# Kernel optimization log

Hardware: AMD Instinct MI355X
Metric: run time of the kernel (lower is better)

The kernel has to match this reference:

```python
import jax, jax.numpy as jnp
import numpy as np

N_NODES = 100000
N_EDGES = 1000000
D_IN = 64
D_OUT = 64


def setup_inputs() -> dict:
    key = jax.random.key(0)
    k_x, k_e, k_w, k_b = jax.random.split(key, 4)
    x = jax.random.normal(k_x, (N_NODES, D_IN), dtype=jnp.float32)
    edge_index = jax.random.randint(k_e, (2, N_EDGES), 0, N_NODES, dtype=jnp.int64)
    # degrees of destination nodes (what the caller is expected to supply);
    # clamp to >=1 to avoid division by zero for isolated nodes
    deg = jax.ops.segment_sum(jnp.ones((N_EDGES,), jnp.float32), edge_index[1], num_segments=N_NODES)
    node_degrees = jnp.maximum(deg, 1.0)
    W = jax.random.normal(k_w, (D_OUT, D_IN), dtype=jnp.float32) * (1.0 / np.sqrt(D_IN))
    b = jax.random.normal(k_b, (D_OUT,), dtype=jnp.float32) * 0.01
    return {"x": x, "edge_index": edge_index, "node_degrees": node_degrees, "W": W, "b": b}


def reference(x, edge_index, node_degrees, W, b):
    # Original does argsort+cumsum+boundary segment-sum; mathematically this is
    # a scatter-add of gathered neighbor features into dst, i.e. a segment sum.
    src, dst = edge_index[0], edge_index[1]
    agg = jax.ops.segment_sum(x[src], dst, num_segments=x.shape[0])  # [N, D_IN]
    mean = agg / node_degrees[:, None]
    return mean @ W.T + b  # [N, D_OUT]
```

## Files before the change

### kernel.cpp

```cpp
#include <hip/hip_runtime.h>


#define D 64
#define BSHIFT 7
#define BNODES (1 << BSHIFT)
#define CAP 2048
#define GTHREADS 512
#define PERTHREAD (CAP / GTHREADS)
#define PXW_THREADS 512
#define MAXB 2048

__device__ inline int detect_stride_block(const unsigned* __restrict__ words,
                                          int E, int* sflag) {
    int t = threadIdx.x;
    if (t < 64) {
        unsigned v = (t < E) ? words[2 * t + 1] : 0u;
        int any = __any(v != 0u);
        if (t == 0) *sflag = any ? 1 : 2;
    }
    __syncthreads();
    return *sflag;
}

__device__ inline unsigned pack_bf16(float a, float b) {
    unsigned ua = __float_as_uint(a), ub = __float_as_uint(b);
    ua += 0x7fffu + ((ua >> 16) & 1u);
    ub += 0x7fffu + ((ub >> 16) & 1u);
    return (ua >> 16) | (ub & 0xffff0000u);
}

__global__ __launch_bounds__(PXW_THREADS, 4) void partition_xw_kernel(
        const unsigned* __restrict__ ewords, int* __restrict__ cursor,
        unsigned* __restrict__ pairs, uint2* __restrict__ spill,
        int* __restrict__ spillCnt,
        const float* __restrict__ x, const float* __restrict__ W,
        unsigned* __restrict__ y2, int E, int N, int nb, int pblocks) {
    __shared__ __align__(16) char smem[52240];
    int t = threadIdx.x;

    if ((int)blockIdx.x < pblocks) {
        int* lhist = (int*)smem;
        int* lbase = lhist + MAXB;
        int* sflag = lbase + MAXB;
        int s = detect_stride_block(ewords, E, sflag);
        int base = blockIdx.x * 8192;
        for (int i = t; i < nb; i += PXW_THREADS) lhist[i] = 0;
        __syncthreads();
        unsigned pv[16]; int bk[16];
        #pragma unroll
        for (int k = 0; k < 16; ++k) {
            int e = base + k * PXW_THREADS + t;
            bk[k] = -1;
            if (e < E) {
                unsigned src = ewords[(size_t)e * s];
                unsigned dst = ewords[((size_t)E + e) * s];
                bk[k] = (int)(dst >> BSHIFT);
                pv[k] = src | ((dst & (BNODES - 1)) << 17);
                atomicAdd(&lhist[bk[k]], 1);
            }
        }
        __syncthreads();
        for (int hb = t; hb < nb; hb += PXW_THREADS) {
            int cc = lhist[hb];
            if (cc) lbase[hb] = atomicAdd(&cursor[hb], cc);
            lhist[hb] = 0;
        }
        __syncthreads();
        #pragma unroll
        for (int k = 0; k < 16; ++k) {
            if (bk[k] >= 0) {
                int lpos = lbase[bk[k]] + atomicAdd(&lhist[bk[k]], 1);
                if (lpos < CAP) {
                    pairs[(size_t)bk[k] * CAP + lpos] = pv[k];
                } else {
                    int si = atomicAdd(spillCnt, 1);
                    unsigned dst = ((unsigned)bk[k] << BSHIFT) | (pv[k] >> 17);
                    spill[si] = make_uint2(pv[k] & 0x1FFFFu, dst);
                }
            }
        }
    } else {
        float* Wt = (float*)smem;
        float* xs = Wt + 64 * 68;
        for (int i = t; i < 64 * 64; i += PXW_THREADS) {
            int o = i >> 6, k = i & 63;
            Wt[k * 68 + o] = W[i];
        }
        int base = ((int)blockIdx.x - pblocks) * 128;
        int row = t >> 4, c4 = (t & 15) * 4;
        #pragma unroll
        for (int r = 0; r < 4; ++r) {
            int nl = row + r * 32;
            int n = base + nl;
            float4 v = {0.f, 0.f, 0.f, 0.f};
            if (n < N) v = *(const float4*)(x + (size_t)n * 64 + c4);
            *(float4*)&xs[nl * 68 + c4] = v;
        }
        __syncthreads();
        int o4 = (t & 15) * 4, nl4 = (t >> 4) * 4;
        float acc[4][4];
        #pragma unroll
        for (int i = 0; i < 4; ++i)
            #pragma unroll
            for (int j = 0; j < 4; ++j) acc[i][j] = 0.f;
        #pragma unroll 2
        for (int k0 = 0; k0 < 64; k0 += 4) {
            float a[4][4], wv[4][4];
            #pragma unroll
            for (int i = 0; i < 4; ++i)
                *(float4*)a[i] = *(const float4*)&xs[(nl4 + i) * 68 + k0];
            #pragma unroll
            for (int dk = 0; dk < 4; ++dk)
                *(float4*)wv[dk] = *(const float4*)&Wt[(k0 + dk) * 68 + o4];
            #pragma unroll
            for (int i = 0; i < 4; ++i)
                #pragma unroll
                for (int j = 0; j < 4; ++j)
                    acc[i][j] += a[i][0] * wv[0][j] + a[i][1] * wv[1][j]
                               + a[i][2] * wv[2][j] + a[i][3] * wv[3][j];
        }
        int n0 = base + nl4;
        #pragma unroll
        for (int i = 0; i < 4; ++i) {
            if (n0 + i < N) {
                uint2 p;
                p.x = pack_bf16(acc[i][0], acc[i][1]);
                p.y = pack_bf16(acc[i][2], acc[i][3]);
                *(uint2*)(y2 + (size_t)(n0 + i) * 32 + (o4 >> 1)) = p;
            }
        }
    }
}

__global__ __launch_bounds__(GTHREADS) void bucket_gather(
        const unsigned* __restrict__ y2, const unsigned* __restrict__ pairs,
        const int* __restrict__ cursor, const uint2* __restrict__ spill,
        const int* __restrict__ spillCnt,
        const float* __restrict__ deg, const float* __restrict__ b,
        float* __restrict__ out, int N) {
    __shared__ unsigned list[CAP];
    __shared__ int cnt[BNODES], st[BNODES], sc[BNODES];
    int t = threadIdx.x;
    int bkt = blockIdx.x, base = bkt << BSHIFT;
    int total = cursor[bkt];
    int cn = total < CAP ? total : CAP;
    int lane = t & 63, w = t >> 6;
    int g = lane >> 4, c = lane & 15;
    float4 bv = ((const float4*)b)[c];

    if (t < BNODES) cnt[t] = 0;
    __syncthreads();
    unsigned pv[PERTHREAD];
    #pragma unroll
    for (int j = 0; j < PERTHREAD; ++j) {
        int i = t + j * GTHREADS;
        pv[j] = (i < cn) ? pairs[(size_t)bkt * CAP + i] : 0xFFFFFFFFu;
        if (i < cn) atomicAdd(&cnt[pv[j] >> 17], 1);
    }
    __syncthreads();
    if (t < BNODES) sc[t] = cnt[t];
    __syncthreads();
    for (int off = 1; off < BNODES; off <<= 1) {
        int v = (t < BNODES && t >= off) ? sc[t - off] : 0;
        __syncthreads();
        if (t < BNODES) sc[t] += v;
        __syncthreads();
    }
    if (t < BNODES) { st[t] = sc[t] - cnt[t]; sc[t] = sc[t] - cnt[t]; }
    __syncthreads();
    #pragma unroll
    for (int j = 0; j < PERTHREAD; ++j) {
        if (pv[j] != 0xFFFFFFFFu) {
            int pos = atomicAdd(&sc[pv[j] >> 17], 1);
            list[pos] = pv[j] & 0x1FFFFu;
        }
    }
    __syncthreads();

    int scnt = *spillCnt;

    for (int nl0 = w * 16; nl0 < w * 16 + 16; nl0 += 4) {
        int mynode = nl0 + g;
        int n = base + mynode;
        int s0 = st[mynode], e1 = s0 + cnt[mynode];
        float ax = 0.f, ay = 0.f, az = 0.f, aw = 0.f;
        float bx = 0.f, by = 0.f, bz = 0.f, bw = 0.f;
        int i = s0;
        for (; i + 1 < e1; i += 2) {
            unsigned s0v = list[i], s1v = list[i + 1];
            uint2 u0 = *(const uint2*)(y2 + (size_t)s0v * 32 + c * 2);
            uint2 u1 = *(const uint2*)(y2 + (size_t)s1v * 32 + c * 2);
            ax += __uint_as_float(u0.x << 16);
            ay += __uint_as_float(u0.x & 0xffff0000u);
            az += __uint_as_float(u0.y << 16);
            aw += __uint_as_float(u0.y & 0xffff0000u);
            bx += __uint_as_float(u1.x << 16);
            by += __uint_as_float(u1.x & 0xffff0000u);
            bz += __uint_as_float(u1.y << 16);
            bw += __uint_as_float(u1.y & 0xffff0000u);
        }
        if (i < e1) {
            unsigned sv = list[i];
            uint2 u = *(const uint2*)(y2 + (size_t)sv * 32 + c * 2);
            ax += __uint_as_float(u.x << 16);
            ay += __uint_as_float(u.x & 0xffff0000u);
            az += __uint_as_float(u.y << 16);
            aw += __uint_as_float(u.y & 0xffff0000u);
        }
        ax += bx; ay += by; az += bz; aw += bw;
        for (int k = 0; k < scnt; ++k) {
            uint2 e = spill[k];
            if ((int)e.y == n) {
                uint2 u = *(const uint2*)(y2 + (size_t)e.x * 32 + c * 2);
                ax += __uint_as_float(u.x << 16);
                ay += __uint_as_float(u.x & 0xffff0000u);
                az += __uint_as_float(u.y << 16);
                aw += __uint_as_float(u.y & 0xffff0000u);
            }
        }
        if (n < N) {
            float invd = 1.0f / deg[n];
            float4 o4 = {ax * invd + bv.x, ay * invd + bv.y,
                         az * invd + bv.z, aw * invd + bv.w};
            *(float4*)(out + (size_t)n * 64 + c * 4) = o4;
        }
    }
}

__global__ __launch_bounds__(256) void scatter_kernel(
        const float* __restrict__ x, const unsigned* __restrict__ ewords,
        float* __restrict__ agg, int E) {
    __shared__ int sflag;
    int s = detect_stride_block(ewords, E, &sflag);
    int gid = blockIdx.x * blockDim.x + threadIdx.x;
    int e = gid >> 4, q = gid & 15;
    if (e >= E) return;
    int src = (int)ewords[(size_t)e * s];
    int dst = (int)ewords[((size_t)E + e) * s];
    const float4 v = *(const float4*)(x + (size_t)src * D + q * 4);
    float* p = agg + (size_t)dst * D + q * 4;
    unsafeAtomicAdd(p + 0, v.x);
    unsafeAtomicAdd(p + 1, v.y);
    unsafeAtomicAdd(p + 2, v.z);
    unsafeAtomicAdd(p + 3, v.w);
}

__global__ __launch_bounds__(256) void gemm_kernel(
        float* __restrict__ inout, const float* __restrict__ deg,
        const float* __restrict__ W, const float* __restrict__ b, int nNodes) {
    __shared__ float Wt[64 * 65];
    __shared__ float rows[4 * 64];
    int t = threadIdx.x;
    for (int i = t; i < 64 * 64; i += 256) {
        int o = i >> 6, k = i & 63;
        Wt[k * 65 + o] = W[i];
    }
    int base = blockIdx.x * 4;
    int nl = t >> 6, o = t & 63;
    int n = base + nl;
    if (n < nNodes) {
        float invd = 1.0f / deg[n];
        rows[nl * 64 + o] = inout[(size_t)n * 64 + o] * invd;
    }
    __syncthreads();
    if (n >= nNodes) return;
    float acc = b[o];
    #pragma unroll
    for (int k = 0; k < 64; ++k)
        acc += rows[nl * 64 + k] * Wt[k * 65 + o];
    inout[(size_t)n * 64 + o] = acc;
}

extern "C" void kernel_launch(void* const* d_in, const int* in_sizes, int n_in,
                              void* d_out, int out_size, void* d_ws, size_t ws_size,
                              hipStream_t stream) {
    const float*    x      = (const float*)d_in[0];
    const unsigned* ewords = (const unsigned*)d_in[1];
    const float*    deg    = (const float*)d_in[2];
    const float*    W      = (const float*)d_in[3];
    const float*    b      = (const float*)d_in[4];
    float*          out    = (float*)d_out;

    const int E = in_sizes[1] / 2;
    const int N = in_sizes[2];
    const int nb = (N + BNODES - 1) >> BSHIFT;

    char* ws = (char*)d_ws;
    size_t curB  = (MAXB + 16) * 4;
    size_t pairB = ((size_t)nb * CAP * 4 + 63) & ~63ull;
    size_t spB   = ((size_t)E * 8 + 63) & ~63ull;
    size_t need  = curB + pairB + spB + (size_t)N * 32 * 4;

    if (ws_size >= need && N < (1 << 17) && nb <= MAXB) {
        int*      cursor   = (int*)ws;
        int*      spillCnt = cursor + MAXB;
        unsigned* pairs    = (unsigned*)(ws + curB);
        uint2*    spill    = (uint2*)(ws + curB + pairB);
        unsigned* y2       = (unsigned*)(ws + curB + pairB + spB);

        hipMemsetAsync(cursor, 0, curB, stream);

        int pblocks  = (E + 8191) / 8192;
        int xwblocks = (N + 127) / 128;
        partition_xw_kernel<<<pblocks + xwblocks, PXW_THREADS, 0, stream>>>(
            ewords, cursor, pairs, spill, spillCnt, x, W, y2, E, N, nb, pblocks);

        bucket_gather<<<nb, GTHREADS, 0, stream>>>(
            y2, pairs, cursor, spill, spillCnt, deg, b, out, N);
    } else {
        hipMemsetAsync(d_out, 0, (size_t)out_size * sizeof(float), stream);
        long long sthreads = (long long)E * 16;
        int sblocks = (int)((sthreads + 255) / 256);
        scatter_kernel<<<sblocks, 256, 0, stream>>>(x, ewords, out, E);
        gemm_kernel<<<(N + 3) / 4, 256, 0, stream>>>(out, deg, W, b, N);
    }
}
```

Before: 139.8 us.

## Shrink gather buckets to 32 nodes with one 16-lane group per node

Bucket size drops from 128 to 32 nodes and per-bucket capacity from 2048 to 512 edges, so each of the 512 threads holds exactly one pair. Each 16-lane group now owns a single node instead of looping over four, and the shared-memory prefix scan over node counts becomes a single-wave shuffle scan. The aim is more, smaller blocks with fewer barriers and more parallelism in the gather. The risk is that a per-bucket capacity of 512 sits close to the expected ~320 edges per bucket, so overflows into the spill list (which every thread scans linearly) may become more frequent. MAXB rises to cover the larger bucket count.

Result: no change. 142.0 us (+1.6%).

```diff
diff --git a/kernel.cpp b/kernel.cpp
--- a/kernel.cpp
+++ b/kernel.cpp
@@ -2,13 +2,12 @@
 
 
 #define D 64
-#define BSHIFT 7
+#define BSHIFT 5
 #define BNODES (1 << BSHIFT)
-#define CAP 2048
+#define CAP 512
 #define GTHREADS 512
-#define PERTHREAD (CAP / GTHREADS)
 #define PXW_THREADS 512
-#define MAXB 2048
+#define MAXB 3328
 
 __device__ inline int detect_stride_block(const unsigned* __restrict__ words,
                                           int E, int* sflag) {
@@ -144,86 +143,74 @@
     int bkt = blockIdx.x, base = bkt << BSHIFT;
     int total = cursor[bkt];
     int cn = total < CAP ? total : CAP;
-    int lane = t & 63, w = t >> 6;
-    int g = lane >> 4, c = lane & 15;
+    int node = t >> 4, c = t & 15;
     float4 bv = ((const float4*)b)[c];
 
     if (t < BNODES) cnt[t] = 0;
     __syncthreads();
-    unsigned pv[PERTHREAD];
-    #pragma unroll
-    for (int j = 0; j < PERTHREAD; ++j) {
-        int i = t + j * GTHREADS;
-        pv[j] = (i < cn) ? pairs[(size_t)bkt * CAP + i] : 0xFFFFFFFFu;
-        if (i < cn) atomicAdd(&cnt[pv[j] >> 17], 1);
-    }
-    __syncthreads();
-    if (t < BNODES) sc[t] = cnt[t];
-    __syncthreads();
-    for (int off = 1; off < BNODES; off <<= 1) {
-        int v = (t < BNODES && t >= off) ? sc[t - off] : 0;
-        __syncthreads();
-        if (t < BNODES) sc[t] += v;
-        __syncthreads();
-    }
-    if (t < BNODES) { st[t] = sc[t] - cnt[t]; sc[t] = sc[t] - cnt[t]; }
-    __syncthreads();
-    #pragma unroll
-    for (int j = 0; j < PERTHREAD; ++j) {
-        if (pv[j] != 0xFFFFFFFFu) {
-            int pos = atomicAdd(&sc[pv[j] >> 17], 1);
-            list[pos] = pv[j] & 0x1FFFFu;
-        }
+    unsigned pv = (t < cn) ? pairs[(size_t)bkt * CAP + t] : 0xFFFFFFFFu;
+    if (pv != 0xFFFFFFFFu) atomicAdd(&cnt[pv >> 17], 1);
+    __syncthreads();
+    if (t < 64) {
+        int v = (t < BNODES) ? cnt[t] : 0;
+        #pragma unroll
+        for (int off = 1; off < BNODES; off <<= 1) {
+            int u = __shfl_up(v, off);
+            if ((t & 63) >= off) v += u;
+        }
+        if (t < BNODES) { st[t] = v - cnt[t]; sc[t] = v - cnt[t]; }
+    }
+    __syncthreads();
+    if (pv != 0xFFFFFFFFu) {
+        int pos = atomicAdd(&sc[pv >> 17], 1);
+        list[pos] = pv & 0x1FFFFu;
     }
     __syncthreads();
 
     int scnt = *spillCnt;
 
-    for (int nl0 = w * 16; nl0 < w * 16 + 16; nl0 += 4) {
-        int mynode = nl0 + g;
-        int n = base + mynode;
-        int s0 = st[mynode], e1 = s0 + cnt[mynode];
-        float ax = 0.f, ay = 0.f, az = 0.f, aw = 0.f;
-        float bx = 0.f, by = 0.f, bz = 0.f, bw = 0.f;
-        int i = s0;
-        for (; i + 1 < e1; i += 2) {
-            unsigned s0v = list[i], s1v = list[i + 1];
-            uint2 u0 = *(const uint2*)(y2 + (size_t)s0v * 32 + c * 2);
-            uint2 u1 = *(const uint2*)(y2 + (size_t)s1v * 32 + c * 2);
-            ax += __uint_as_float(u0.x << 16);
-            ay += __uint_as_float(u0.x & 0xffff0000u);
-            az += __uint_as_float(u0.y << 16);
-            aw += __uint_as_float(u0.y & 0xffff0000u);
-            bx += __uint_as_float(u1.x << 16);
-            by += __uint_as_float(u1.x & 0xffff0000u);
-            bz += __uint_as_float(u1.y << 16);
-            bw += __uint_as_float(u1.y & 0xffff0000u);
-        }
-        if (i < e1) {
-            unsigned sv = list[i];
-            uint2 u = *(const uint2*)(y2 + (size_t)sv * 32 + c * 2);
+    int n = base + node;
+    int s0 = st[node], e1 = s0 + cnt[node];
+    float ax = 0.f, ay = 0.f, az = 0.f, aw = 0.f;
+    float bx = 0.f, by = 0.f, bz = 0.f, bw = 0.f;
+    int i = s0;
+    for (; i + 1 < e1; i += 2) {
+        unsigned s0v = list[i], s1v = list[i + 1];
+        uint2 u0 = *(const uint2*)(y2 + (size_t)s0v * 32 + c * 2);
+        uint2 u1 = *(const uint2*)(y2 + (size_t)s1v * 32 + c * 2);
+        ax += __uint_as_float(u0.x << 16);
+        ay += __uint_as_float(u0.x & 0xffff0000u);
+        az += __uint_as_float(u0.y << 16);
+        aw += __uint_as_float(u0.y & 0xffff0000u);
+        bx += __uint_as_float(u1.x << 16);
+        by += __uint_as_float(u1.x & 0xffff0000u);
+        bz += __uint_as_float(u1.y << 16);
+        bw += __uint_as_float(u1.y & 0xffff0000u);
+    }
+    if (i < e1) {
+        unsigned sv = list[i];
+        uint2 u = *(const uint2*)(y2 + (size_t)sv * 32 + c * 2);
+        ax += __uint_as_float(u.x << 16);
+        ay += __uint_as_float(u.x & 0xffff0000u);
+        az += __uint_as_float(u.y << 16);
+        aw += __uint_as_float(u.y & 0xffff0000u);
+    }
+    ax += bx; ay += by; az += bz; aw += bw;
+    for (int k = 0; k < scnt; ++k) {
+        uint2 e = spill[k];
+        if ((int)e.y == n) {
+            uint2 u = *(const uint2*)(y2 + (size_t)e.x * 32 + c * 2);
             ax += __uint_as_float(u.x << 16);
             ay += __uint_as_float(u.x & 0xffff0000u);
             az += __uint_as_float(u.y << 16);
             aw += __uint_as_float(u.y & 0xffff0000u);
         }
-        ax += bx; ay += by; az += bz; aw += bw;
-        for (int k = 0; k < scnt; ++k) {
-            uint2 e = spill[k];
-            if ((int)e.y == n) {
-                uint2 u = *(const uint2*)(y2 + (size_t)e.x * 32 + c * 2);
-                ax += __uint_as_float(u.x << 16);
-                ay += __uint_as_float(u.x & 0xffff0000u);
-                az += __uint_as_float(u.y << 16);
-                aw += __uint_as_float(u.y & 0xffff0000u);
-            }
-        }
-        if (n < N) {
-            float invd = 1.0f / deg[n];
-            float4 o4 = {ax * invd + bv.x, ay * invd + bv.y,
-                         az * invd + bv.z, aw * invd + bv.w};
-            *(float4*)(out + (size_t)n * 64 + c * 4) = o4;
-        }
+    }
+    if (n < N) {
+        float invd = 1.0f / deg[n];
+        float4 o4 = {ax * invd + bv.x, ay * invd + bv.y,
+                     az * invd + bv.z, aw * invd + bv.w};
+        *(float4*)(out + (size_t)n * 64 + c * 4) = o4;
     }
 }
 
```

## Halve gather bucket size and widen per-thread loads to 16 bytes

Applied to the files above, without the earlier changes.

Buckets shrink from 128 to 64 destination nodes with capacity 1024, so twice as many blocks run the gather kernel. Each thread now handles one node and 8 channels with uint4 loads, eight threads per node, where before it looped over 4 nodes with uint2 loads. The shared-memory prefix scan over the 64 node counts becomes a single-wavefront shuffle scan, which drops several block-wide barriers. In exchange, high-degree nodes now sit on a single thread group, and the spill path may be hit more often when a bucket exceeds the smaller capacity.

After: 139.8 us. About the same (-0.0%).

```diff
diff --git a/kernel.cpp b/kernel.cpp
--- a/kernel.cpp
+++ b/kernel.cpp
@@ -2,9 +2,9 @@
 
 
 #define D 64
-#define BSHIFT 7
+#define BSHIFT 6
 #define BNODES (1 << BSHIFT)
-#define CAP 2048
+#define CAP 1024
 #define GTHREADS 512
 #define PERTHREAD (CAP / GTHREADS)
 #define PXW_THREADS 512
@@ -144,9 +144,9 @@
     int bkt = blockIdx.x, base = bkt << BSHIFT;
     int total = cursor[bkt];
     int cn = total < CAP ? total : CAP;
-    int lane = t & 63, w = t >> 6;
-    int g = lane >> 4, c = lane & 15;
-    float4 bv = ((const float4*)b)[c];
+    int node = t >> 3, c = t & 7;
+    float4 bv0 = ((const float4*)b)[c * 2];
+    float4 bv1 = ((const float4*)b)[c * 2 + 1];
 
     if (t < BNODES) cnt[t] = 0;
     __syncthreads();
@@ -155,18 +155,18 @@
     for (int j = 0; j < PERTHREAD; ++j) {
         int i = t + j * GTHREADS;
         pv[j] = (i < cn) ? pairs[(size_t)bkt * CAP + i] : 0xFFFFFFFFu;
-        if (i < cn) atomicAdd(&cnt[pv[j] >> 17], 1);
-    }
-    __syncthreads();
-    if (t < BNODES) sc[t] = cnt[t];
-    __syncthreads();
-    for (int off = 1; off < BNODES; off <<= 1) {
-        int v = (t < BNODES && t >= off) ? sc[t - off] : 0;
-        __syncthreads();
-        if (t < BNODES) sc[t] += v;
-        __syncthreads();
-    }
-    if (t < BNODES) { st[t] = sc[t] - cnt[t]; sc[t] = sc[t] - cnt[t]; }
+        if (pv[j] != 0xFFFFFFFFu) atomicAdd(&cnt[pv[j] >> 17], 1);
+    }
+    __syncthreads();
+    if (t < 64) {
+        int v = cnt[t];
+        #pragma unroll
+        for (int off = 1; off < 64; off <<= 1) {
+            int u = __shfl_up(v, off);
+            if (t >= off) v += u;
+        }
+        st[t] = v - cnt[t]; sc[t] = v - cnt[t];
+    }
     __syncthreads();
     #pragma unroll
     for (int j = 0; j < PERTHREAD; ++j) {
@@ -179,51 +179,70 @@
 
     int scnt = *spillCnt;
 
-    for (int nl0 = w * 16; nl0 < w * 16 + 16; nl0 += 4) {
-        int mynode = nl0 + g;
-        int n = base + mynode;
-        int s0 = st[mynode], e1 = s0 + cnt[mynode];
-        float ax = 0.f, ay = 0.f, az = 0.f, aw = 0.f;
-        float bx = 0.f, by = 0.f, bz = 0.f, bw = 0.f;
-        int i = s0;
-        for (; i + 1 < e1; i += 2) {
-            unsigned s0v = list[i], s1v = list[i + 1];
-            uint2 u0 = *(const uint2*)(y2 + (size_t)s0v * 32 + c * 2);
-            uint2 u1 = *(const uint2*)(y2 + (size_t)s1v * 32 + c * 2);
-            ax += __uint_as_float(u0.x << 16);
-            ay += __uint_as_float(u0.x & 0xffff0000u);
-            az += __uint_as_float(u0.y << 16);
-            aw += __uint_as_float(u0.y & 0xffff0000u);
-            bx += __uint_as_float(u1.x << 16);
-            by += __uint_as_float(u1.x & 0xffff0000u);
-            bz += __uint_as_float(u1.y << 16);
-            bw += __uint_as_float(u1.y & 0xffff0000u);
-        }
-        if (i < e1) {
-            unsigned sv = list[i];
-            uint2 u = *(const uint2*)(y2 + (size_t)sv * 32 + c * 2);
-            ax += __uint_as_float(u.x << 16);
-            ay += __uint_as_float(u.x & 0xffff0000u);
-            az += __uint_as_float(u.y << 16);
-            aw += __uint_as_float(u.y & 0xffff0000u);
-        }
-        ax += bx; ay += by; az += bz; aw += bw;
-        for (int k = 0; k < scnt; ++k) {
-            uint2 e = spill[k];
-            if ((int)e.y == n) {
-                uint2 u = *(const uint2*)(y2 + (size_t)e.x * 32 + c * 2);
-                ax += __uint_as_float(u.x << 16);
-                ay += __uint_as_float(u.x & 0xffff0000u);
-                az += __uint_as_float(u.y << 16);
-                aw += __uint_as_float(u.y & 0xffff0000u);
-            }
-        }
-        if (n < N) {
-            float invd = 1.0f / deg[n];
-            float4 o4 = {ax * invd + bv.x, ay * invd + bv.y,
-                         az * invd + bv.z, aw * invd + bv.w};
-            *(float4*)(out + (size_t)n * 64 + c * 4) = o4;
-        }
+    int n = base + node;
+    int s0 = st[node], e1 = s0 + cnt[node];
+    float a0 = 0.f, a1 = 0.f, a2 = 0.f, a3 = 0.f;
+    float a4 = 0.f, a5 = 0.f, a6 = 0.f, a7 = 0.f;
+    float b0 = 0.f, b1 = 0.f, b2 = 0.f, b3 = 0.f;
+    float b4 = 0.f, b5 = 0.f, b6 = 0.f, b7 = 0.f;
+    int i = s0;
+    for (; i + 1 < e1; i += 2) {
+        unsigned s0v = list[i], s1v = list[i + 1];
+        uint4 u0 = *(const uint4*)(y2 + (size_t)s0v * 32 + c * 4);
+        uint4 u1 = *(const uint4*)(y2 + (size_t)s1v * 32 + c * 4);
+        a0 += __uint_as_float(u0.x << 16);
+        a1 += __uint_as_float(u0.x & 0xffff0000u);
+        a2 += __uint_as_float(u0.y << 16);
+        a3 += __uint_as_float(u0.y & 0xffff0000u);
+        a4 += __uint_as_float(u0.z << 16);
+        a5 += __uint_as_float(u0.z & 0xffff0000u);
+        a6 += __uint_as_float(u0.w << 16);
+        a7 += __uint_as_float(u0.w & 0xffff0000u);
+        b0 += __uint_as_float(u1.x << 16);
+        b1 += __uint_as_float(u1.x & 0xffff0000u);
+        b2 += __uint_as_float(u1.y << 16);
+        b3 += __uint_as_float(u1.y & 0xffff0000u);
+        b4 += __uint_as_float(u1.z << 16);
+        b5 += __uint_as_float(u1.z & 0xffff0000u);
+        b6 += __uint_as_float(u1.w << 16);
+        b7 += __uint_as_float(u1.w & 0xffff0000u);
+    }
+    if (i < e1) {
+        unsigned sv = list[i];
+        uint4 u = *(const uint4*)(y2 + (size_t)sv * 32 + c * 4);
+        a0 += __uint_as_float(u.x << 16);
+        a1 += __uint_as_float(u.x & 0xffff0000u);
+        a2 += __uint_as_float(u.y << 16);
+        a3 += __uint_as_float(u.y & 0xffff0000u);
+        a4 += __uint_as_float(u.z << 16);
+        a5 += __uint_as_float(u.z & 0xffff0000u);
+        a6 += __uint_as_float(u.w << 16);
+        a7 += __uint_as_float(u.w & 0xffff0000u);
+    }
+    a0 += b0; a1 += b1; a2 += b2; a3 += b3;
+    a4 += b4; a5 += b5; a6 += b6; a7 += b7;
+    for (int k = 0; k < scnt; ++k) {
+        uint2 e = spill[k];
+        if ((int)e.y == n) {
+            uint4 u = *(const uint4*)(y2 + (size_t)e.x * 32 + c * 4);
+            a0 += __uint_as_float(u.x << 16);
+            a1 += __uint_as_float(u.x & 0xffff0000u);
+            a2 += __uint_as_float(u.y << 16);
+            a3 += __uint_as_float(u.y & 0xffff0000u);
+            a4 += __uint_as_float(u.z << 16);
+            a5 += __uint_as_float(u.z & 0xffff0000u);
+            a6 += __uint_as_float(u.w << 16);
+            a7 += __uint_as_float(u.w & 0xffff0000u);
+        }
+    }
+    if (n < N) {
+        float invd = 1.0f / deg[n];
+        float4 o0 = {a0 * invd + bv0.x, a1 * invd + bv0.y,
+                     a2 * invd + bv0.z, a3 * invd + bv0.w};
+        float4 o1 = {a4 * invd + bv1.x, a5 * invd + bv1.y,
+                     a6 * invd + bv1.z, a7 * invd + bv1.w};
+        *(float4*)(out + (size_t)n * 64 + c * 8) = o0;
+        *(float4*)(out + (size_t)n * 64 + c * 8 + 4) = o1;
     }
 }
 
```
